# Kernel optimization log

Measured on AMD Instinct MI355X. Metric: run time of the kernel, lower is better.

The kernel has to match this reference:

```python
import jax, jax.numpy as jnp
import numpy as np

# dims: S sets, M max items, DIN input feat, DM model dim (= head_size), H heads, L layers
S, M, DIN, DM, H, DH, L = 48, 128, 128, 128, 4, 128, 2
ALPHA = 0.3  # tf.keras.layers.LeakyReLU default alpha


def gelu(x):
    return jax.nn.gelu(x, approximate=False)  # tf.nn.gelu default is exact


def leaky(x):
    return jnp.where(x >= 0, x, ALPHA * x)


def set_norm(x, size):
    # masked per-set normalization over all items*features; pad rows (feature-sum == 0) are zeroed
    d = x.shape[-1]
    mask = (jnp.sum(x, axis=-1, keepdims=True) != 0).astype(x.dtype)  # [S,M,1]
    denom = size * d  # [S]
    mean = jnp.sum(x, axis=(1, 2)) / denom
    diff = x - mean[:, None, None]
    var = jnp.sum(jnp.square(diff) * mask, axis=(1, 2)) / denom
    return diff / (jnp.sqrt(var)[:, None, None] + 1e-8) * mask


def masked_softmax(s):
    # original masks by *nonzero score values*, not an additive bias
    mask = s != 0
    e = jnp.where(mask, jnp.exp(s - jnp.max(s, axis=-1, keepdims=True)), 0.0)
    return e / (jnp.sum(e, axis=-1, keepdims=True) + 1e-10)


def attention(x, wq, wk, wv, wh):
    split = lambda z: z.reshape(z.shape[0], z.shape[1], H, DH).transpose(0, 2, 1, 3)  # [S,H,M,D]
    q, k, v = split(x @ wq), split(x @ wk), split(x @ wv)
    s = jnp.einsum('shmd,shnd->shmn', q, k) / np.float32(np.sqrt(DH))
    a = masked_softmax(s)
    o = jnp.einsum('shmn,shnd->shmd', a, v).transpose(0, 2, 1, 3).reshape(x.shape[0], x.shape[1], H * DH)
    return o @ wh


def forward(x, size, W_proj, Wq, Wk, Wv, Wh, Wfc, Wc, w2):
    mask = (jnp.sum(x != 0, axis=-1, keepdims=True) > 0).astype(x.dtype)  # [S,M,1] valid-item mask
    h = gelu(x @ W_proj) * mask
    for l in range(L):
        a = attention(h, Wq[l], Wk[l], Wv[l], Wh[l]) * mask
        h = set_norm(h + a, size)
        f = gelu(h @ Wfc[l]) * mask
        h = set_norm(h + f, size)
    # cross_set_score (tuple branch, x == y): pairwise per-head set scores
    z = (h @ Wc).reshape(h.shape[0], h.shape[1], H, DH).transpose(0, 2, 1, 3)  # [S,H,M,D]
    s = leaky(jnp.einsum('jhmd,ihnd->jihmn', z, z) / np.float32(np.sqrt(DH)))  # [Sy,Sx,H,My,Mx]
    scores = jnp.sum(s, axis=(-1, -2)) / size[None, :, None] / np.float32(M)  # [Sy,Sx,H]
    return scores @ w2  # [Sy,Sx,1]


def setup_inputs() -> dict:
    key = jax.random.key(0)
    ks = jax.random.split(key, 10)
    x = jax.random.normal(ks[0], (S, M, DIN), jnp.float32)
    x_size = jax.random.randint(ks[1], (S,), 1, M + 1, jnp.int32)
    x = x * (jnp.arange(M)[None, :] < x_size[:, None])[:, :, None]  # zero-pad beyond set size
    sc = lambda n: np.float32(1.0 / np.sqrt(n))
    W_proj = jax.random.normal(ks[2], (DIN, DM), jnp.float32) * sc(DIN)
    Wq = jax.random.normal(ks[3], (L, DM, H * DH), jnp.float32) * sc(DM)
    Wk = jax.random.normal(ks[4], (L, DM, H * DH), jnp.float32) * sc(DM)
    Wv = jax.random.normal(ks[5], (L, DM, H * DH), jnp.float32) * sc(DM)
    Wh = jax.random.normal(ks[6], (L, H * DH, DM), jnp.float32) * sc(H * DH)
    Wfc = jax.random.normal(ks[7], (L, DM, DM), jnp.float32) * sc(DM)
    Wc = jax.random.normal(ks[8], (DM, H * DH), jnp.float32) * sc(DM)
    w2 = jax.random.normal(ks[9], (H, 1), jnp.float32) * sc(H)
    return dict(x=x, x_size=x_size, W_proj=W_proj, Wq=Wq, Wk=Wk, Wv=Wv, Wh=Wh, Wfc=Wfc, Wc=Wc, w2=w2)


def reference(x, x_size, W_proj, Wq, Wk, Wv, Wh, Wfc, Wc, w2):
    size = jnp.maximum(x_size, 1).astype(jnp.float32)
    return forward(x, size, W_proj, Wq, Wk, Wv, Wh, Wfc, Wc, w2)
```

## Files before the change

kernel.cpp:

```cpp
#include <hip/hip_runtime.h>
#include <hip/hip_bf16.h>
#include <math.h>

typedef unsigned short u16;
typedef short bf16x8 __attribute__((ext_vector_type(8)));
typedef float f32x4 __attribute__((ext_vector_type(4)));
typedef float f32x16 __attribute__((ext_vector_type(16)));

__device__ __forceinline__ u16 f2b(float f){
  union { float f; unsigned u; } c; c.f = f;
  unsigned u = c.u;
  unsigned r = (u + 0x7fffu + ((u >> 16) & 1u)) >> 16;
  return (u16)r;
}
__device__ __forceinline__ unsigned pack2(float a, float b){
  return (unsigned)f2b(a) | ((unsigned)f2b(b) << 16);
}
__device__ __forceinline__ float gelu_f(float x){
  return 0.5f * x * (1.0f + erff(x * 0.70710678118654752f));
}

__global__ __launch_bounds__(256) void prep_weights(
    const float* __restrict__ Wproj, const float* __restrict__ Wq,
    const float* __restrict__ Wk,    const float* __restrict__ Wv,
    const float* __restrict__ Whp,   const float* __restrict__ Wfc,
    const float* __restrict__ Wc,    u16* __restrict__ wT)
{
  __shared__ __align__(16) u16 Ah[128*136];
  __shared__ __align__(16) u16 Bv[128*136];
  int bid = blockIdx.x, tid = threadIdx.x;
  if (bid < 312) {
    int cid = bid * 256 + tid;
    if (cid >= 34816 && cid < 67584) return;
    int region, lh = 0, c;
    if      (cid < 2048)  { region = 0; c = cid; }
    else if (cid < 18432) { int o = cid - 2048;  region = 1; lh = o >> 11; c = o & 2047; }
    else if (cid < 34816) { int o = cid - 18432; region = 2; lh = o >> 11; c = o & 2047; }
    else if (cid < 71680) { int o = cid - 67584; region = 5; lh = o >> 11; c = o & 2047; }
    else                  { int o = cid - 71680; region = 6; lh = o >> 11; c = o & 2047; }
    int l16 = c & 15, quad = (c >> 4) & 3, ks = (c >> 6) & 3, nt = c >> 8;
    int n = nt * 16 + l16, kb = ks * 32 + quad * 8;
    int l = lh >> 2, hh = lh & 3;
    const float rs = 0.08838834764831845f;
    u16 tmp[8];
#pragma unroll
    for (int e = 0; e < 8; ++e) {
      int k = kb + e;
      float v;
      switch (region) {
        case 0: v = Wproj[k * 128 + n]; break;
        case 1: v = Wq[l * 65536 + k * 512 + hh * 128 + n] * rs; break;
        case 2: v = Wk[l * 65536 + k * 512 + hh * 128 + n]; break;
        case 5: v = Wfc[lh * 16384 + k * 128 + n]; break;
        default: v = Wc[k * 512 + lh * 128 + n]; break;
      }
      tmp[e] = f2b(v);
    }
    *(uint4*)(wT + (size_t)cid * 8) = *(uint4*)tmp;
    return;
  }
  int lhb = bid - 312; int l = lhb >> 2, hh = lhb & 3;
#pragma unroll
  for (int it = 0; it < 64; ++it) {
    int idx = it * 256 + tid;
    int a = idx & 127, b = idx >> 7;
    Ah[a * 136 + b] = f2b(Whp[l * 65536 + (hh * 128 + b) * 128 + a]);
    Bv[b * 136 + a] = f2b(Wv[l * 65536 + b * 512 + hh * 128 + a]);
  }
  __syncthreads();
  int wv = tid >> 6, lane = tid & 63, quad = lane >> 4, l16 = lane & 15;
  f32x4 acc[2][8] = {};
  for (int ks = 0; ks < 4; ++ks) {
    bf16x8 aF[2], bF[8];
#pragma unroll
    for (int i = 0; i < 2; ++i)
      aF[i] = *(const bf16x8*)(Ah + ((wv*2+i)*16 + l16)*136 + ks*32 + quad*8);
#pragma unroll
    for (int n = 0; n < 8; ++n)
      bF[n] = *(const bf16x8*)(Bv + (n*16 + l16)*136 + ks*32 + quad*8);
#pragma unroll
    for (int i = 0; i < 2; ++i)
#pragma unroll
      for (int n = 0; n < 8; ++n)
        acc[i][n] = __builtin_amdgcn_mfma_f32_16x16x32_bf16(aF[i], bF[n], acc[i][n], 0, 0, 0);
  }
  size_t base = 278528 + (size_t)lhb * 16384;
#pragma unroll
  for (int i = 0; i < 2; ++i)
#pragma unroll
    for (int n2 = 0; n2 < 8; ++n2)
#pragma unroll
      for (int g = 0; g < 4; ++g) {
        int n = (wv*2+i)*16 + quad*4 + g;
        int k = n2*16 + l16;
        wT[base + (size_t)((((n>>4)*4 + (k>>5))*4 + ((k>>3)&3))*16 + (n&15))*8 + (k&7)]
            = f2b(acc[i][n2][g]);
      }
}

__device__ __forceinline__ void gemm_g(const u16* A, const u16* __restrict__ Bg,
    f32x4 (*acc)[4], int wr, int wc, int quad, int l16, int lane){
#pragma unroll
  for (int ks = 0; ks < 4; ++ks){
    bf16x8 aF[2], bF[4];
#pragma unroll
    for (int i = 0; i < 2; ++i)
      aF[i] = *(const bf16x8*)(A + ((wr*2+i)*16 + l16)*136 + ks*32 + quad*8);
#pragma unroll
    for (int n = 0; n < 4; ++n)
      bF[n] = *(const bf16x8*)(Bg + ((size_t)(((wc*4+n)*4 + ks)*64 + lane))*8);
#pragma unroll
    for (int i = 0; i < 2; ++i)
#pragma unroll
      for (int n = 0; n < 4; ++n)
        acc[i][n] = __builtin_amdgcn_mfma_f32_16x16x32_bf16(aF[i], bF[n], acc[i][n], 0, 0, 0);
  }
}

__device__ __forceinline__ void write_rm(u16* dst, f32x4 (*acc)[4],
                                         int wr, int wc, int quad, int l16){
#pragma unroll
  for (int i = 0; i < 2; ++i)
#pragma unroll
    for (int n = 0; n < 4; ++n)
#pragma unroll
      for (int g = 0; g < 4; ++g)
        dst[((wr*2+i)*16 + quad*4 + g)*136 + (wc*4+n)*16 + l16] = f2b(acc[i][n][g]);
}

__device__ __forceinline__ void write_tr(u16* dst, f32x4 (*acc)[4],
                                         int wr, int wc, int quad, int l16){
#pragma unroll
  for (int i = 0; i < 2; ++i)
#pragma unroll
    for (int n = 0; n < 4; ++n)
#pragma unroll
      for (int g = 0; g < 4; ++g)
        dst[((wc*4+n)*16 + l16)*136 + (wr*2+i)*16 + quad*4 + g] = f2b(acc[i][n][g]);
}

__device__ __forceinline__ void block_reduce2(float &s1, float &s2,
                                              float* red, int wv, int lane){
#pragma unroll
  for (int off = 1; off < 64; off <<= 1){
    s1 += __shfl_xor(s1, off, 64);
    s2 += __shfl_xor(s2, off, 64);
  }
  if (lane == 0){ red[wv*2] = s1; red[wv*2+1] = s2; }
  __syncthreads();
  s1 = red[0]+red[2]+red[4]+red[6]+red[8]+red[10]+red[12]+red[14];
  s2 = red[1]+red[3]+red[5]+red[7]+red[9]+red[11]+red[13]+red[15];
  __syncthreads();
}

__global__ __launch_bounds__(512, 2) void trunk(
    const float* __restrict__ x, const int* __restrict__ xsize,
    const u16* __restrict__ wT, u16* __restrict__ zg)
{
  __shared__ __align__(16) u16 hA[128*136];
  __shared__ __align__(16) u16 qP[128*136];
  __shared__ __align__(16) u16 kB[128*136];
  __shared__ __align__(16) u16 vB[128*136];
  __shared__ float svalid[128];
  __shared__ float red[16];
  int tid = threadIdx.x;
  int wv = tid >> 6, lane = tid & 63, quad = lane >> 4, l16 = lane & 15;
  int wr = wv >> 1, wc = wv & 1;
  int s = blockIdx.x;
  int sz = xsize[s]; if (sz < 1) sz = 1;
  int Mt = (sz + 15) >> 4, Mk = (sz + 31) >> 5;
  float den = (float)sz * 128.0f;

#pragma unroll
  for (int it = 0; it < 4; ++it) {
    int ch = tid + it * 512; int r = ch >> 4, cc = ch & 15;
    const float* p = x + ((size_t)s * 128 + r) * 128 + cc * 8;
    float4 u0 = *(const float4*)p, u1 = *(const float4*)(p + 4);
    int nz = (u0.x!=0.f)|(u0.y!=0.f)|(u0.z!=0.f)|(u0.w!=0.f)|
             (u1.x!=0.f)|(u1.y!=0.f)|(u1.z!=0.f)|(u1.w!=0.f);
    nz |= __shfl_xor(nz,1,64); nz |= __shfl_xor(nz,2,64);
    nz |= __shfl_xor(nz,4,64); nz |= __shfl_xor(nz,8,64);
    if ((tid & 15) == 0) svalid[r] = nz ? 1.f : 0.f;
    uint4 w;
    w.x = pack2(u0.x,u0.y); w.y = pack2(u0.z,u0.w);
    w.z = pack2(u1.x,u1.y); w.w = pack2(u1.z,u1.w);
    *(uint4*)(hA + r*136 + cc*8) = w;
  }
  __syncthreads();

  f32x4 hR[2][4];
  {
    f32x4 acc[2][4] = {};
    gemm_g(hA, wT, acc, wr, wc, quad, l16, lane);
    __syncthreads();
#pragma unroll
    for (int i = 0; i < 2; ++i)
#pragma unroll
      for (int n = 0; n < 4; ++n)
#pragma unroll
        for (int g = 0; g < 4; ++g) {
          int row = (wr*2+i)*16 + quad*4 + g;
          float gg = gelu_f(acc[i][n][g]) * svalid[row];
          hR[i][n][g] = gg;
          hA[row*136 + (wc*4+n)*16 + l16] = f2b(gg);
        }
    __syncthreads();
  }

#pragma unroll 1
  for (int l = 0; l < 2; ++l) {
    f32x4 aR[2][4] = {};
#pragma unroll 1
    for (int hh = 0; hh < 4; ++hh) {
      int lh = l * 4 + hh;
      {
        f32x4 qa[2][4] = {};
        gemm_g(hA, wT + 16384 + lh*16384, qa, wr, wc, quad, l16, lane);
        write_rm(qP, qa, wr, wc, quad, l16);
      }
      {
        f32x4 ka[2][4] = {};
        gemm_g(hA, wT + 147456 + lh*16384, ka, wr, wc, quad, l16, lane);
        write_rm(kB, ka, wr, wc, quad, l16);
      }
      {
        f32x4 va[2][4] = {};
        gemm_g(hA, wT + 278528 + lh*16384, va, wr, wc, quad, l16, lane);
        write_tr(vB, va, wr, wc, quad, l16);
      }
      __syncthreads();
      if (wv < Mt) {
        bf16x8 qA[4];
#pragma unroll
        for (int ks = 0; ks < 4; ++ks)
          qA[ks] = *(const bf16x8*)(qP + (wv*16 + l16)*136 + ks*32 + quad*8);
        f32x4 sacc[8] = {};
#pragma unroll
        for (int ks = 0; ks < 4; ++ks) {
          bf16x8 bF[8];
#pragma unroll
          for (int j = 0; j < 8; ++j)
            if (j < Mt) bF[j] = *(const bf16x8*)(kB + (j*16+l16)*136 + ks*32 + quad*8);
#pragma unroll
          for (int j = 0; j < 8; ++j)
            if (j < Mt) sacc[j] = __builtin_amdgcn_mfma_f32_16x16x32_bf16(qA[ks], bF[j], sacc[j], 0, 0, 0);
        }
        for (int g = 0; g < 4; ++g) {
          float vals[8]; float rmax = -1e30f;
#pragma unroll
          for (int j = 0; j < 8; ++j)
            if (j < Mt) {
              float v = sacc[j][g];
              vals[j] = v;
              rmax = fmaxf(rmax, v);
            }
          for (int off = 1; off < 16; off <<= 1) rmax = fmaxf(rmax, __shfl_xor(rmax, off, 64));
          if (sz < 128) rmax = fmaxf(rmax, 0.0f);
          float rsum = 0.f;
#pragma unroll
          for (int j = 0; j < 8; ++j)
            if (j < Mt) {
              float e = (vals[j] != 0.0f) ? expf(vals[j] - rmax) : 0.0f;
              vals[j] = e; rsum += e;
            }
          for (int off = 1; off < 16; off <<= 1) rsum += __shfl_xor(rsum, off, 64);
          float inv = 1.0f / (rsum + 1e-10f);
#pragma unroll
          for (int j = 0; j < 8; ++j)
            if (j < Mt) sacc[j][g] = vals[j] * inv;
        }
#pragma unroll
        for (int j = 0; j < 8; ++j)
          if (j < Mt)
#pragma unroll
            for (int g = 0; g < 4; ++g)
              qP[(wv*16 + quad*4 + g)*136 + j*16 + l16] = f2b(sacc[j][g]);
      }
      __syncthreads();
#pragma unroll
      for (int i = 0; i < 2; ++i) {
        int mtile = wr*2 + i;
        if (mtile < Mt) {
          for (int ks = 0; ks < Mk; ++ks) {
            bf16x8 aF = *(const bf16x8*)(qP + (mtile*16 + l16)*136 + ks*32 + quad*8);
            bf16x8 bF[4];
#pragma unroll
            for (int n = 0; n < 4; ++n)
              bF[n] = *(const bf16x8*)(vB + ((wc*4+n)*16+l16)*136 + ks*32 + quad*8);
#pragma unroll
            for (int n = 0; n < 4; ++n)
              aR[i][n] = __builtin_amdgcn_mfma_f32_16x16x32_bf16(aF, bF[n], aR[i][n], 0, 0, 0);
          }
        }
      }
      __syncthreads();
    }

    {
      float ls1 = 0.f, ls2 = 0.f;
#pragma unroll
      for (int i = 0; i < 2; ++i)
#pragma unroll
        for (int n = 0; n < 4; ++n)
#pragma unroll
          for (int g = 0; g < 4; ++g) {
            int row = (wr*2+i)*16 + quad*4 + g;
            float u = hR[i][n][g] + aR[i][n][g] * svalid[row];
            hR[i][n][g] = u;
            ls1 += u; ls2 += u * u;
          }
      block_reduce2(ls1, ls2, red, wv, lane);
      float mean = ls1 / den;
      float var = ls2 / den - mean * mean; if (var < 0.f) var = 0.f;
      float inv = 1.0f / (sqrtf(var) + 1e-8f);
#pragma unroll
      for (int i = 0; i < 2; ++i)
#pragma unroll
        for (int n = 0; n < 4; ++n)
#pragma unroll
          for (int g = 0; g < 4; ++g) {
            int row = (wr*2+i)*16 + quad*4 + g;
            float hn = (hR[i][n][g] - mean) * inv * svalid[row];
            hR[i][n][g] = hn;
            hA[row*136 + (wc*4+n)*16 + l16] = f2b(hn);
          }
      __syncthreads();
    }
    {
      f32x4 fa[2][4] = {};
      gemm_g(hA, wT + 540672 + l*16384, fa, wr, wc, quad, l16, lane);
      float ls1 = 0.f, ls2 = 0.f;
#pragma unroll
      for (int i = 0; i < 2; ++i)
#pragma unroll
        for (int n = 0; n < 4; ++n)
#pragma unroll
          for (int g = 0; g < 4; ++g) {
            int row = (wr*2+i)*16 + quad*4 + g;
            float u = hR[i][n][g] + gelu_f(fa[i][n][g]) * svalid[row];
            hR[i][n][g] = u;
            ls1 += u; ls2 += u * u;
          }
      block_reduce2(ls1, ls2, red, wv, lane);
      float mean = ls1 / den;
      float var = ls2 / den - mean * mean; if (var < 0.f) var = 0.f;
      float inv = 1.0f / (sqrtf(var) + 1e-8f);
#pragma unroll
      for (int i = 0; i < 2; ++i)
#pragma unroll
        for (int n = 0; n < 4; ++n)
#pragma unroll
          for (int g = 0; g < 4; ++g) {
            int row = (wr*2+i)*16 + quad*4 + g;
            float hn = (hR[i][n][g] - mean) * inv * svalid[row];
            hR[i][n][g] = hn;
            hA[row*136 + (wc*4+n)*16 + l16] = f2b(hn);
          }
      __syncthreads();
    }
  }

#pragma unroll 1
  for (int hh = 0; hh < 4; ++hh) {
    f32x4 za[2][4] = {};
    gemm_g(hA, wT + 573440 + hh*16384, za, wr, wc, quad, l16, lane);
    u16* zb = zg + (((size_t)s*4 + hh) << 14);
#pragma unroll
    for (int i = 0; i < 2; ++i)
#pragma unroll
      for (int n = 0; n < 4; ++n)
#pragma unroll
        for (int g = 0; g < 4; ++g) {
          int row = (wr*2+i)*16 + quad*4 + g;
          int col = (wc*4+n)*16 + l16;
          zb[(size_t)(((row>>5)*8 + (col>>4))*512 + ((col>>3)&1)*256
                      + (row&31)*8 + (col&7))] = f2b(za[i][n][g]);
        }
  }
}

__global__ __launch_bounds__(256) void cross_kernel(
    const u16* __restrict__ zg, float* __restrict__ Tbuf, const int* __restrict__ xsize)
{
  __shared__ float red[4];
  int tid = threadIdx.x, wave = tid >> 6, lane = tid & 63;
  int t4 = blockIdx.x;
  int pr = t4 >> 2, hh = t4 & 3;
  float jf = (97.0f - sqrtf(9409.0f - 8.0f * (float)pr)) * 0.5f;
  int j = (int)jf; if (j > 47) j = 47; if (j < 0) j = 0;
  while (j > 0 && j * 48 - (j * (j - 1)) / 2 > pr) --j;
  while ((j + 1) * 48 - ((j + 1) * j) / 2 <= pr) ++j;
  int i = j + pr - (j * 48 - (j * (j - 1)) / 2);
  int sj = xsize[j]; if (sj < 1) sj = 1;
  int si = xsize[i]; if (si < 1) si = 1;
  int MjT = (sj + 31) >> 5, MiT = (si + 31) >> 5;
  const u16* zj = zg + (((size_t)j * 4 + hh) << 14);
  const u16* zi = zg + (((size_t)i * 4 + hh) << 14);
  int gA = (wave >> 1) * 2, gB = (wave & 1) * 2;
  bool a0 = gA < MjT, a1 = (gA + 1) < MjT;
  bool b0 = gB < MiT, b1 = (gB + 1) < MiT;
  f32x16 acc[2][2] = {};
  if ((a0 || a1) && (b0 || b1)) {
#pragma unroll
    for (int ks = 0; ks < 8; ++ks) {
      bf16x8 aF[2], bF[2];
      if (a0) aF[0] = *(const bf16x8*)(zj + (size_t)((gA    )*8 + ks)*512 + lane*8);
      if (a1) aF[1] = *(const bf16x8*)(zj + (size_t)((gA + 1)*8 + ks)*512 + lane*8);
      if (b0) bF[0] = *(const bf16x8*)(zi + (size_t)((gB    )*8 + ks)*512 + lane*8);
      if (b1) bF[1] = *(const bf16x8*)(zi + (size_t)((gB + 1)*8 + ks)*512 + lane*8);
      if (a0 && b0) acc[0][0] = __builtin_amdgcn_mfma_f32_32x32x16_bf16(aF[0], bF[0], acc[0][0], 0, 0, 0);
      if (a0 && b1) acc[0][1] = __builtin_amdgcn_mfma_f32_32x32x16_bf16(aF[0], bF[1], acc[0][1], 0, 0, 0);
      if (a1 && b0) acc[1][0] = __builtin_amdgcn_mfma_f32_32x32x16_bf16(aF[1], bF[0], acc[1][0], 0, 0, 0);
      if (a1 && b1) acc[1][1] = __builtin_amdgcn_mfma_f32_32x32x16_bf16(aF[1], bF[1], acc[1][1], 0, 0, 0);
    }
  }
  float s1 = 0.f, s2 = 0.f;
#pragma unroll
  for (int ii = 0; ii < 2; ++ii)
#pragma unroll
    for (int jj = 0; jj < 2; ++jj) {
      bool tact = (ii ? a1 : a0) && (jj ? b1 : b0);
      if (tact)
#pragma unroll
        for (int r = 0; r < 16; ++r) {
          float a = acc[ii][jj][r];
          s1 += a; s2 += fabsf(a);
        }
    }
  const float rs = 0.08838834764831845f;
  float tp = rs * (0.65f * s1 + 0.35f * s2);
  for (int off = 1; off < 64; off <<= 1) tp += __shfl_xor(tp, off, 64);
  if (lane == 0) red[wave] = tp;
  __syncthreads();
  if (tid == 0)
    Tbuf[((j * 48 + i) << 2) + hh] = red[0] + red[1] + red[2] + red[3];
}

__global__ __launch_bounds__(256) void final_kernel(
    const float* __restrict__ Tbuf, const float* __restrict__ w2,
    const int* __restrict__ xsize, float* __restrict__ out)
{
  int idx = blockIdx.x * 256 + threadIdx.x;
  if (idx >= 2304) return;
  int a = idx / 48, b = idx - a * 48;
  int j = a < b ? a : b, i = a < b ? b : a;
  float t = 0.f;
  for (int h = 0; h < 4; ++h) t += Tbuf[((j * 48 + i) << 2) + h] * w2[h];
  int szb = xsize[b]; if (szb < 1) szb = 1;
  out[idx] = t / ((float)szb * 128.0f);
}

extern "C" void kernel_launch(void* const* d_in, const int* in_sizes, int n_in,
                              void* d_out, int out_size, void* d_ws, size_t ws_size,
                              hipStream_t stream)
{
  const float* x     = (const float*)d_in[0];
  const int*   xsize = (const int*)d_in[1];
  const float* Wproj = (const float*)d_in[2];
  const float* Wq    = (const float*)d_in[3];
  const float* Wk    = (const float*)d_in[4];
  const float* Wv    = (const float*)d_in[5];
  const float* Whp   = (const float*)d_in[6];
  const float* Wfc   = (const float*)d_in[7];
  const float* Wc    = (const float*)d_in[8];
  const float* w2    = (const float*)d_in[9];
  float* out = (float*)d_out;

  char* ws = (char*)d_ws;
  size_t off = 0;
  auto alloc = [&](size_t bytes) -> char* {
    char* p = ws + off;
    off += (bytes + 255) & ~(size_t)255;
    return p;
  };
  u16*   wT   = (u16*)  alloc(638976 * 2);
  float* Tbuf = (float*)alloc(9216 * 4);
  u16*   zg   = (u16*)  alloc((size_t)3145728 * 2);

  prep_weights<<<320, 256, 0, stream>>>(Wproj, Wq, Wk, Wv, Whp, Wfc, Wc, wT);
  trunk<<<48, 512, 0, stream>>>(x, xsize, wT, zg);
  cross_kernel<<<4704, 256, 0, stream>>>(zg, Tbuf, xsize);
  final_kernel<<<9, 256, 0, stream>>>(Tbuf, w2, xsize, out);
}
```

Measured before the change: 230.7 us.

## Defer set-norm into next GEMM epilogue using precomputed weight column sums

Instead of normalising h before each GEMM, the trunk feeds the un-normalised residual into the GEMM and applies the mean and scale correction in the epilogue, using per-column weight sums computed in prep_weights (extra blocks). This removes separate normalisation passes and one barrier-separated reduction round per layer, letting the FC GEMM start right after the first reduction. It adds extra csum shared memory (15 KB), more epilogue arithmetic, and numeric differences because the bf16 inputs are no longer normalised before rounding.

```diff
diff --git a/kernel.cpp b/kernel.cpp
--- a/kernel.cpp
+++ b/kernel.cpp
@@ -13,6 +13,9 @@
   unsigned r = (u + 0x7fffu + ((u >> 16) & 1u)) >> 16;
   return (u16)r;
 }
+__device__ __forceinline__ float b2f(u16 h){
+  union { unsigned u; float f; } c; c.u = ((unsigned)h) << 16; return c.f;
+}
 __device__ __forceinline__ unsigned pack2(float a, float b){
   return (unsigned)f2b(a) | ((unsigned)f2b(b) << 16);
 }
@@ -24,11 +27,13 @@
     const float* __restrict__ Wproj, const float* __restrict__ Wq,
     const float* __restrict__ Wk,    const float* __restrict__ Wv,
     const float* __restrict__ Whp,   const float* __restrict__ Wfc,
-    const float* __restrict__ Wc,    u16* __restrict__ wT)
+    const float* __restrict__ Wc,    u16* __restrict__ wT,
+    float* __restrict__ csumG)
 {
   __shared__ __align__(16) u16 Ah[128*136];
   __shared__ __align__(16) u16 Bv[128*136];
   int bid = blockIdx.x, tid = threadIdx.x;
+  const float rs = 0.08838834764831845f;
   if (bid < 312) {
     int cid = bid * 256 + tid;
     if (cid >= 34816 && cid < 67584) return;
@@ -41,7 +46,6 @@
     int l16 = c & 15, quad = (c >> 4) & 3, ks = (c >> 6) & 3, nt = c >> 8;
     int n = nt * 16 + l16, kb = ks * 32 + quad * 8;
     int l = lh >> 2, hh = lh & 3;
-    const float rs = 0.08838834764831845f;
     u16 tmp[8];
 #pragma unroll
     for (int e = 0; e < 8; ++e) {
@@ -59,6 +63,34 @@
     *(uint4*)(wT + (size_t)cid * 8) = *(uint4*)tmp;
     return;
   }
+  if (bid >= 320) {
+    int cb = bid - 320;
+    if (tid >= 128) return;
+    int n = tid;
+    float s = 0.f;
+    if (cb < 8) {
+      int l = cb >> 2, hh = cb & 3;
+      for (int k = 0; k < 128; ++k)
+        s += b2f(f2b(Wq[l * 65536 + k * 512 + hh * 128 + n] * rs));
+      csumG[cb * 128 + n] = s;
+    } else if (cb < 16) {
+      int lh = cb - 8, l = lh >> 2, hh = lh & 3;
+      for (int k = 0; k < 128; ++k)
+        s += b2f(f2b(Wk[l * 65536 + k * 512 + hh * 128 + n]));
+      csumG[1024 + lh * 128 + n] = s;
+    } else if (cb < 18) {
+      int l = cb - 16;
+      for (int k = 0; k < 128; ++k)
+        s += b2f(f2b(Wfc[l * 16384 + k * 128 + n]));
+      csumG[3072 + l * 128 + n] = s;
+    } else {
+      int hh = cb - 18;
+      for (int k = 0; k < 128; ++k)
+        s += b2f(f2b(Wc[k * 512 + hh * 128 + n]));
+      csumG[3328 + hh * 128 + n] = s;
+    }
+    return;
+  }
   int lhb = bid - 312; int l = lhb >> 2, hh = lhb & 3;
 #pragma unroll
   for (int it = 0; it < 64; ++it) {
@@ -96,6 +128,20 @@
         wT[base + (size_t)((((n>>4)*4 + (k>>5))*4 + ((k>>3)&3))*16 + (n&15))*8 + (k&7)]
             = f2b(acc[i][n2][g]);
       }
+#pragma unroll
+  for (int i = 0; i < 2; ++i)
+#pragma unroll
+    for (int g = 0; g < 4; ++g) {
+      float s = 0.f;
+#pragma unroll
+      for (int n2 = 0; n2 < 8; ++n2) s += b2f(f2b(acc[i][n2][g]));
+      s += __shfl_xor(s, 1, 64); s += __shfl_xor(s, 2, 64);
+      s += __shfl_xor(s, 4, 64); s += __shfl_xor(s, 8, 64);
+      if (l16 == 0) {
+        int n = (wv*2+i)*16 + quad*4 + g;
+        csumG[2048 + lhb * 128 + n] = s;
+      }
+    }
 }
 
 __device__ __forceinline__ void gemm_g(const u16* A, const u16* __restrict__ Bg,
@@ -117,52 +163,52 @@
   }
 }
 
-__device__ __forceinline__ void write_rm(u16* dst, f32x4 (*acc)[4],
-                                         int wr, int wc, int quad, int l16){
+__device__ __forceinline__ void epi_rm(u16* dst, f32x4 (*acc)[4],
+    const float* cs, float mu, float inv, const float* sval,
+    int wr, int wc, int quad, int l16){
 #pragma unroll
   for (int i = 0; i < 2; ++i)
 #pragma unroll
-    for (int n = 0; n < 4; ++n)
-#pragma unroll
-      for (int g = 0; g < 4; ++g)
-        dst[((wr*2+i)*16 + quad*4 + g)*136 + (wc*4+n)*16 + l16] = f2b(acc[i][n][g]);
-}
-
-__device__ __forceinline__ void write_tr(u16* dst, f32x4 (*acc)[4],
-                                         int wr, int wc, int quad, int l16){
+    for (int n = 0; n < 4; ++n) {
+      int col = (wc*4+n)*16 + l16;
+      float c = mu * cs[col];
+#pragma unroll
+      for (int g = 0; g < 4; ++g) {
+        int row = (wr*2+i)*16 + quad*4 + g;
+        dst[row*136 + col] = f2b((acc[i][n][g] - c) * inv * sval[row]);
+      }
+    }
+}
+
+__device__ __forceinline__ void epi_tr(u16* dst, f32x4 (*acc)[4],
+    const float* cs, float mu, float inv, const float* sval,
+    int wr, int wc, int quad, int l16){
 #pragma unroll
   for (int i = 0; i < 2; ++i)
 #pragma unroll
-    for (int n = 0; n < 4; ++n)
-#pragma unroll
-      for (int g = 0; g < 4; ++g)
-        dst[((wc*4+n)*16 + l16)*136 + (wr*2+i)*16 + quad*4 + g] = f2b(acc[i][n][g]);
-}
-
-__device__ __forceinline__ void block_reduce2(float &s1, float &s2,
-                                              float* red, int wv, int lane){
-#pragma unroll
-  for (int off = 1; off < 64; off <<= 1){
-    s1 += __shfl_xor(s1, off, 64);
-    s2 += __shfl_xor(s2, off, 64);
-  }
-  if (lane == 0){ red[wv*2] = s1; red[wv*2+1] = s2; }
-  __syncthreads();
-  s1 = red[0]+red[2]+red[4]+red[6]+red[8]+red[10]+red[12]+red[14];
-  s2 = red[1]+red[3]+red[5]+red[7]+red[9]+red[11]+red[13]+red[15];
-  __syncthreads();
+    for (int n = 0; n < 4; ++n) {
+      int col = (wc*4+n)*16 + l16;
+      float c = mu * cs[col];
+#pragma unroll
+      for (int g = 0; g < 4; ++g) {
+        int row = (wr*2+i)*16 + quad*4 + g;
+        dst[col*136 + row] = f2b((acc[i][n][g] - c) * inv * sval[row]);
+      }
+    }
 }
 
 __global__ __launch_bounds__(512, 2) void trunk(
     const float* __restrict__ x, const int* __restrict__ xsize,
-    const u16* __restrict__ wT, u16* __restrict__ zg)
+    const u16* __restrict__ wT, const float* __restrict__ csumG,
+    u16* __restrict__ zg)
 {
   __shared__ __align__(16) u16 hA[128*136];
   __shared__ __align__(16) u16 qP[128*136];
   __shared__ __align__(16) u16 kB[128*136];
   __shared__ __align__(16) u16 vB[128*136];
   __shared__ float svalid[128];
-  __shared__ float red[16];
+  __shared__ float red[32];
+  __shared__ float sCs[3840];
   int tid = threadIdx.x;
   int wv = tid >> 6, lane = tid & 63, quad = lane >> 4, l16 = lane & 15;
   int wr = wv >> 1, wc = wv & 1;
@@ -170,6 +216,8 @@
   int sz = xsize[s]; if (sz < 1) sz = 1;
   int Mt = (sz + 15) >> 4, Mk = (sz + 31) >> 5;
   float den = (float)sz * 128.0f;
+
+  for (int idx = tid; idx < 3840; idx += 512) sCs[idx] = csumG[idx];
 
 #pragma unroll
   for (int it = 0; it < 4; ++it) {
@@ -206,6 +254,7 @@
         }
     __syncthreads();
   }
+  float cur_mu = 0.f, cur_inv = 1.f;
 
 #pragma unroll 1
   for (int l = 0; l < 2; ++l) {
@@ -216,17 +265,17 @@
       {
         f32x4 qa[2][4] = {};
         gemm_g(hA, wT + 16384 + lh*16384, qa, wr, wc, quad, l16, lane);
-        write_rm(qP, qa, wr, wc, quad, l16);
+        epi_rm(qP, qa, sCs + lh*128, cur_mu, cur_inv, svalid, wr, wc, quad, l16);
       }
       {
         f32x4 ka[2][4] = {};
         gemm_g(hA, wT + 147456 + lh*16384, ka, wr, wc, quad, l16, lane);
-        write_rm(kB, ka, wr, wc, quad, l16);
+        epi_rm(kB, ka, sCs + 1024 + lh*128, cur_mu, cur_inv, svalid, wr, wc, quad, l16);
       }
       {
         f32x4 va[2][4] = {};
         gemm_g(hA, wT + 278528 + lh*16384, va, wr, wc, quad, l16, lane);
-        write_tr(vB, va, wr, wc, quad, l16);
+        epi_tr(vB, va, sCs + 2048 + lh*128, cur_mu, cur_inv, svalid, wr, wc, quad, l16);
       }
       __syncthreads();
       if (wv < Mt) {
@@ -297,7 +346,8 @@
     }
 
     {
-      float ls1 = 0.f, ls2 = 0.f;
+      f32x4 u1[2][4];
+      float a1 = 0.f, a2 = 0.f;
 #pragma unroll
       for (int i = 0; i < 2; ++i)
 #pragma unroll
@@ -305,31 +355,58 @@
 #pragma unroll
           for (int g = 0; g < 4; ++g) {
             int row = (wr*2+i)*16 + quad*4 + g;
-            float u = hR[i][n][g] + aR[i][n][g] * svalid[row];
-            hR[i][n][g] = u;
-            ls1 += u; ls2 += u * u;
+            float hn = (hR[i][n][g]);
+            float u = hn + aR[i][n][g] * svalid[row];
+            u1[i][n][g] = u;
+            a1 += u; a2 += u * u;
+            qP[row*136 + (wc*4+n)*16 + l16] = f2b(u);
           }
-      block_reduce2(ls1, ls2, red, wv, lane);
-      float mean = ls1 / den;
-      float var = ls2 / den - mean * mean; if (var < 0.f) var = 0.f;
-      float inv = 1.0f / (sqrtf(var) + 1e-8f);
+#pragma unroll
+      for (int off = 1; off < 64; off <<= 1) {
+        a1 += __shfl_xor(a1, off, 64);
+        a2 += __shfl_xor(a2, off, 64);
+      }
+      if (lane == 0) { red[wv*2] = a1; red[wv*2+1] = a2; }
+      __syncthreads();
+      float S1 = red[0]+red[2]+red[4]+red[6]+red[8]+red[10]+red[12]+red[14];
+      float S2 = red[1]+red[3]+red[5]+red[7]+red[9]+red[11]+red[13]+red[15];
+      float mu1 = S1 / den;
+      float var1 = S2 / den - mu1 * mu1; if (var1 < 0.f) var1 = 0.f;
+      float inv1 = 1.0f / (sqrtf(var1) + 1e-8f);
+      f32x4 fa[2][4] = {};
+      gemm_g(qP, wT + 540672 + l*16384, fa, wr, wc, quad, l16, lane);
+      const float* csF = sCs + 3072 + l*128;
+      float b1 = 0.f, b2 = 0.f;
 #pragma unroll
       for (int i = 0; i < 2; ++i)
 #pragma unroll
-        for (int n = 0; n < 4; ++n)
+        for (int n = 0; n < 4; ++n) {
+          int col = (wc*4+n)*16 + l16;
+          float c = mu1 * csF[col];
 #pragma unroll
           for (int g = 0; g < 4; ++g) {
             int row = (wr*2+i)*16 + quad*4 + g;
-            float hn = (hR[i][n][g] - mean) * inv * svalid[row];
-            hR[i][n][g] = hn;
-            hA[row*136 + (wc*4+n)*16 + l16] = f2b(hn);
+            float vl = svalid[row];
+            float f = (fa[i][n][g] - c) * inv1 * vl;
+            float hn1 = (u1[i][n][g] - mu1) * inv1 * vl;
+            float u2 = hn1 + gelu_f(f) * vl;
+            u1[i][n][g] = u2;
+            b1 += u2; b2 += u2 * u2;
+            hA[row*136 + col] = f2b(u2);
           }
+        }
+#pragma unroll
+      for (int off = 1; off < 64; off <<= 1) {
+        b1 += __shfl_xor(b1, off, 64);
+        b2 += __shfl_xor(b2, off, 64);
+      }
+      if (lane == 0) { red[16 + wv*2] = b1; red[17 + wv*2] = b2; }
       __syncthreads();
-    }
-    {
-      f32x4 fa[2][4] = {};
-      gemm_g(hA, wT + 540672 + l*16384, fa, wr, wc, quad, l16, lane);
-      float ls1 = 0.f, ls2 = 0.f;
+      float T1 = red[16]+red[18]+red[20]+red[22]+red[24]+red[26]+red[28]+red[30];
+      float T2 = red[17]+red[19]+red[21]+red[23]+red[25]+red[27]+red[29]+red[31];
+      float mu2 = T1 / den;
+      float var2 = T2 / den - mu2 * mu2; if (var2 < 0.f) var2 = 0.f;
+      float inv2 = 1.0f / (sqrtf(var2) + 1e-8f);
 #pragma unroll
       for (int i = 0; i < 2; ++i)
 #pragma unroll
@@ -337,26 +414,9 @@
 #pragma unroll
           for (int g = 0; g < 4; ++g) {
             int row = (wr*2+i)*16 + quad*4 + g;
-            float u = hR[i][n][g] + gelu_f(fa[i][n][g]) * svalid[row];
-            hR[i][n][g] = u;
-            ls1 += u; ls2 += u * u;
+            hR[i][n][g] = (u1[i][n][g] - mu2) * inv2 * svalid[row];
           }
-      block_reduce2(ls1, ls2, red, wv, lane);
-      float mean = ls1 / den;
-      float var = ls2 / den - mean * mean; if (var < 0.f) var = 0.f;
-      float inv = 1.0f / (sqrtf(var) + 1e-8f);
-#pragma unroll
-      for (int i = 0; i < 2; ++i)
-#pragma unroll
-        for (int n = 0; n < 4; ++n)
-#pragma unroll
-          for (int g = 0; g < 4; ++g) {
-            int row = (wr*2+i)*16 + quad*4 + g;
-            float hn = (hR[i][n][g] - mean) * inv * svalid[row];
-            hR[i][n][g] = hn;
-            hA[row*136 + (wc*4+n)*16 + l16] = f2b(hn);
-          }
-      __syncthreads();
+      cur_mu = mu2; cur_inv = inv2;
     }
   }
 
@@ -364,18 +424,22 @@
   for (int hh = 0; hh < 4; ++hh) {
     f32x4 za[2][4] = {};
     gemm_g(hA, wT + 573440 + hh*16384, za, wr, wc, quad, l16, lane);
+    const float* csC = sCs + 3328 + hh*128;
     u16* zb = zg + (((size_t)s*4 + hh) << 14);
 #pragma unroll
     for (int i = 0; i < 2; ++i)
 #pragma unroll
-      for (int n = 0; n < 4; ++n)
+      for (int n = 0; n < 4; ++n) {
+        int col = (wc*4+n)*16 + l16;
+        float c = cur_mu * csC[col];
 #pragma unroll
         for (int g = 0; g < 4; ++g) {
           int row = (wr*2+i)*16 + quad*4 + g;
-          int col = (wc*4+n)*16 + l16;
+          float v = (za[i][n][g] - c) * cur_inv * svalid[row];
           zb[(size_t)(((row>>5)*8 + (col>>4))*512 + ((col>>3)&1)*256
-                      + (row&31)*8 + (col&7))] = f2b(za[i][n][g]);
-        }
+                      + (row&31)*8 + (col&7))] = f2b(v);
+        }
+      }
   }
 }
 
@@ -473,12 +537,13 @@
     off += (bytes + 255) & ~(size_t)255;
     return p;
   };
-  u16*   wT   = (u16*)  alloc(638976 * 2);
-  float* Tbuf = (float*)alloc(9216 * 4);
-  u16*   zg   = (u16*)  alloc((size_t)3145728 * 2);
-
-  prep_weights<<<320, 256, 0, stream>>>(Wproj, Wq, Wk, Wv, Whp, Wfc, Wc, wT);
-  trunk<<<48, 512, 0, stream>>>(x, xsize, wT, zg);
+  u16*   wT    = (u16*)  alloc(638976 * 2);
+  float* csumG = (float*)alloc(3840 * 4);
+  float* Tbuf  = (float*)alloc(9216 * 4);
+  u16*   zg    = (u16*)  alloc((size_t)3145728 * 2);
+
+  prep_weights<<<342, 256, 0, stream>>>(Wproj, Wq, Wk, Wv, Whp, Wfc, Wc, wT, csumG);
+  trunk<<<48, 512, 0, stream>>>(x, xsize, wT, csumG, zg);
   cross_kernel<<<4704, 256, 0, stream>>>(zg, Tbuf, xsize);
   final_kernel<<<9, 256, 0, stream>>>(Tbuf, w2, xsize, out);
 }
```

Measured after the change: 245.1 us. +6.2%, slower.
